# Optimization experiments

Hardware: AMD Instinct MI355X
Metric: run time of the kernel (lower is better)

## Reference

```python
import jax, jax.numpy as jnp
import numpy as np

D, K = 512, 32


def setup_inputs() -> dict:
    key = jax.random.key(0)
    k1, k2, k3 = jax.random.split(key, 3)
    X = jax.random.normal(k1, (8, D, 128, 128), dtype=jnp.float32)
    std1 = 1.0 / (K * D) ** 0.5
    codewords = jax.random.uniform(k2, (K, D), dtype=jnp.float32, minval=-std1, maxval=std1)
    scale = jax.random.uniform(k3, (K,), dtype=jnp.float32, minval=-1.0, maxval=0.0)
    return {"X": X, "codewords": codewords, "scale": scale}


def reference(X, codewords, scale):
    B = X.shape[0]
    # [B, D, H, W] -> [B, N, D]
    Xf = X.reshape(B, D, -1).transpose(0, 2, 1)
    # scaled L2: s_k * ||x_i - d_k||^2, expanded to avoid [B,N,K,D] residuals
    x2 = jnp.sum(Xf * Xf, axis=-1, keepdims=True)            # [B, N, 1]
    c2 = jnp.sum(codewords * codewords, axis=-1)              # [K]
    xc = jnp.einsum('bnd,kd->bnk', Xf, codewords)             # [B, N, K]
    sl = scale * (x2 - 2.0 * xc + c2)                         # [B, N, K]
    A = jax.nn.softmax(sl, axis=2)                            # [B, N, K]
    # E[b,k,d] = sum_n A[b,n,k] * (X[b,n,d] - C[k,d])
    E = jnp.einsum('bnk,bnd->bkd', A, Xf) - jnp.sum(A, axis=1)[..., None] * codewords
    return E
```

## Files before the change

kernel.cpp:

```cpp
#include <hip/hip_runtime.h>
#include <stdint.h>

#define B_ 8
#define D_ 512
#define N_ 16384
#define K_ 32

typedef __attribute__((ext_vector_type(8))) short short8;
typedef __attribute__((ext_vector_type(16))) float f32x16;

union F8 { short8 v; unsigned short s[8]; uint32_t u[4]; uint4 q; };

__device__ __forceinline__ uint32_t bfpack2(float lo, float hi) {
    uint32_t a = __float_as_uint(lo);
    uint32_t b = __float_as_uint(hi);
    a += 0x7FFFu + ((a >> 16) & 1u);
    b += 0x7FFFu + ((b >> 16) & 1u);
    return (a >> 16) | (b & 0xFFFF0000u);
}

__launch_bounds__(256, 2)
__global__ void encode_kernel(const float* __restrict__ X,
                              const float* __restrict__ Cg,
                              const float* __restrict__ scale,
                              float* __restrict__ acc,
                              float* __restrict__ aSumAcc)
{
    __shared__ uint32_t xsTw[D_ * 20];
    __shared__ float    lgp[4][32][33];
    __shared__ uint32_t A_ldsw[K_ * 20];
    __shared__ float4   x2tmp[32][8];
    __shared__ float    mxs[32], invs[32];
    __shared__ float    scs[K_], c2s[K_];
    __shared__ float    c2tmp[K_][9];

    unsigned short* xsTs  = (unsigned short*)xsTw;
    unsigned short* A_lds = (unsigned short*)A_ldsw;

    const int tid = threadIdx.x;
    const int l   = tid & 63;
    const int w   = __builtin_amdgcn_readfirstlane(tid >> 6);
    const int lc  = l & 31;
    const int nh  = l >> 5;
    const int b     = blockIdx.x >> 6;
    const int chunk = blockIdx.x & 63;

    {
        int k = tid >> 3, dg = tid & 7;
        const float* cr = Cg + k * D_ + dg * 64;
        float s2 = 0.f;
#pragma unroll
        for (int i = 0; i < 16; ++i) {
            float4 v = *(const float4*)(cr + i * 4);
            s2 += v.x * v.x + v.y * v.y + v.z * v.z + v.w * v.w;
        }
        c2tmp[k][dg] = s2;
        if (tid < K_) scs[tid] = scale[tid];
    }
    __syncthreads();
    if (tid < K_) {
        float s = 0.f;
#pragma unroll
        for (int dg = 0; dg < 8; ++dg) s += c2tmp[tid][dg];
        c2s[tid] = s;
    }

    F8 cfr[8];
#pragma unroll
    for (int ss = 0; ss < 8; ++ss) {
        int d0 = (8 * w + ss) * 16 + nh * 8;
        const float* cp = Cg + lc * D_ + d0;
        float4 a  = *(const float4*)(cp);
        float4 bq = *(const float4*)(cp + 4);
        cfr[ss].u[0] = bfpack2(a.x, a.y);
        cfr[ss].u[1] = bfpack2(a.z, a.w);
        cfr[ss].u[2] = bfpack2(bq.x, bq.y);
        cfr[ss].u[3] = bfpack2(bq.z, bq.w);
    }

    f32x16 eacc[4];
#pragma unroll
    for (int ti = 0; ti < 4; ++ti)
#pragma unroll
        for (int r = 0; r < 16; ++r) eacc[ti][r] = 0.f;
    float aSumReg = 0.f;

    const int o  = tid >> 3;
    const int nq = tid & 7;
    const size_t xbase = (size_t)b * D_ * N_ + (size_t)chunk * 256;

    for (int t = 0; t < 8; ++t) {
        __syncthreads();

        {
            const float* Xp = X + xbase + t * 32 + nq * 4;
            float4 x2a; x2a.x = x2a.y = x2a.z = x2a.w = 0.f;
#pragma unroll
            for (int r = 0; r < 16; ++r) {
                int d = o + 32 * r;
                float4 v = *(const float4*)(Xp + (size_t)d * N_);
                x2a.x += v.x * v.x; x2a.y += v.y * v.y;
                x2a.z += v.z * v.z; x2a.w += v.w * v.w;
                uint2 p;
                p.x = bfpack2(v.x, v.y);
                p.y = bfpack2(v.z, v.w);
                *(uint2*)&xsTw[d * 20 + nq * 2] = p;
            }
            x2tmp[o][nq] = x2a;
        }
        __syncthreads();

        f32x16 lacc;
#pragma unroll
        for (int r = 0; r < 16; ++r) lacc[r] = 0.f;
#pragma unroll
        for (int ss = 0; ss < 8; ++ss) {
            int d0 = (8 * w + ss) * 16 + nh * 8;
            F8 af;
#pragma unroll
            for (int j = 0; j < 8; ++j)
                af.s[j] = xsTs[(d0 + j) * 40 + lc];
            lacc = __builtin_amdgcn_mfma_f32_32x32x16_bf16(af.v, cfr[ss].v, lacc, 0, 0, 0);
        }
#pragma unroll
        for (int r = 0; r < 16; ++r)
            lgp[w][(r & 3) + 8 * (r >> 2) + 4 * nh][lc] = lacc[r];
        __syncthreads();

        if (w == 0 && l < 32) {
            int n = l;
            float x2v = 0.f;
            const float* xf = (const float*)x2tmp;
#pragma unroll
            for (int oo = 0; oo < 32; ++oo) x2v += xf[oo * 32 + n];
            float lg[K_];
            float m = -3.0e38f;
#pragma unroll
            for (int k = 0; k < K_; ++k) {
                float xc = lgp[0][n][k] + lgp[1][n][k] + lgp[2][n][k] + lgp[3][n][k];
                float sl = scs[k] * (x2v - 2.f * xc + c2s[k]);
                lg[k] = sl;
                m = fmaxf(m, sl);
            }
            float s = 0.f;
#pragma unroll
            for (int k = 0; k < K_; ++k) s += __expf(lg[k] - m);
            mxs[n] = m;
            invs[n] = 1.f / s;
#pragma unroll
            for (int k = 0; k < K_; ++k) lgp[0][n][k] = lg[k];
        }
        __syncthreads();

        if (w == 0) {
            int k = lc;
#pragma unroll
            for (int i = 0; i < 16; i += 2) {
                int n = nh * 16 + i;
                float e0 = __expf(lgp[0][n][k]     - mxs[n])     * invs[n];
                float e1 = __expf(lgp[0][n + 1][k] - mxs[n + 1]) * invs[n + 1];
                aSumReg += e0 + e1;
                A_ldsw[k * 20 + (n >> 1)] = bfpack2(e0, e1);
            }
        }
        __syncthreads();

#pragma unroll
        for (int ti = 0; ti < 4; ++ti) {
            int dcol = (4 * w + ti) * 32 + lc;
#pragma unroll
            for (int ns = 0; ns < 2; ++ns) {
                F8 af, bf;
                af.q = *(const uint4*)&A_lds[lc * 40 + ns * 16 + nh * 8];
                bf.q = *(const uint4*)&xsTs[dcol * 40 + ns * 16 + nh * 8];
                eacc[ti] = __builtin_amdgcn_mfma_f32_32x32x16_bf16(af.v, bf.v, eacc[ti], 0, 0, 0);
            }
        }
    }

    float* accB = acc + (size_t)b * (K_ * D_);
#pragma unroll
    for (int ti = 0; ti < 4; ++ti) {
        int d = (4 * w + ti) * 32 + lc;
#pragma unroll
        for (int r = 0; r < 16; ++r) {
            int k = (r & 3) + 8 * (r >> 2) + 4 * nh;
            unsafeAtomicAdd(&accB[k * D_ + d], eacc[ti][r]);
        }
    }
    if (w == 0) unsafeAtomicAdd(&aSumAcc[b * K_ + lc], aSumReg);
}

__global__ void finish_kernel(const float* __restrict__ acc,
                              const float* __restrict__ aSumAcc,
                              const float* __restrict__ Cg,
                              float* __restrict__ out)
{
    int idx = blockIdx.x * 256 + threadIdx.x;
    int kd = idx & (K_ * D_ - 1);
    int b  = idx >> 14;
    int k  = kd >> 9;
    out[idx] = acc[idx] - aSumAcc[(b << 5) + k] * Cg[kd];
}

extern "C" void kernel_launch(void* const* d_in, const int* in_sizes, int n_in,
                              void* d_out, int out_size, void* d_ws, size_t ws_size,
                              hipStream_t stream)
{
    const float* X  = (const float*)d_in[0];
    const float* C  = (const float*)d_in[1];
    const float* sc = (const float*)d_in[2];
    float* out = (float*)d_out;

    float* acc     = (float*)d_ws;
    float* aSumAcc = acc + B_ * K_ * D_;

    hipMemsetAsync(d_ws, 0, (size_t)(B_ * K_ * D_ + B_ * K_) * sizeof(float), stream);
    encode_kernel<<<B_ * 64, 256, 0, stream>>>(X, C, sc, acc, aSumAcc);
    finish_kernel<<<(B_ * K_ * D_) / 256, 256, 0, stream>>>(acc, aSumAcc, C, out);
}
```

Baseline: 392.9 us.

## Parallelize softmax across all waves and replace global atomics with partial buffers

The softmax step previously ran on a single wave; it is now spread over all four waves, with 8 lanes per row working together through shuffle reductions. The x2 reduction moves from LDS to wave shuffles. The E accumulator no longer uses global float atomics: each block writes a private partial of 64KB, and finish_kernel sums the 64 chunk partials per batch. This removes serial softmax work and atomic contention. In exchange it adds about 32MB of partial-buffer writes and reads.

```diff
diff --git a/kernel.cpp b/kernel.cpp
--- a/kernel.cpp
+++ b/kernel.cpp
@@ -23,16 +23,16 @@
 __global__ void encode_kernel(const float* __restrict__ X,
                               const float* __restrict__ Cg,
                               const float* __restrict__ scale,
-                              float* __restrict__ acc,
+                              float* __restrict__ part,
                               float* __restrict__ aSumAcc)
 {
     __shared__ uint32_t xsTw[D_ * 20];
-    __shared__ float    lgp[4][32][33];
+    __shared__ float    lgp[4][32][36];
     __shared__ uint32_t A_ldsw[K_ * 20];
-    __shared__ float4   x2tmp[32][8];
-    __shared__ float    mxs[32], invs[32];
+    __shared__ float    x2p[4][32];
     __shared__ float    scs[K_], c2s[K_];
     __shared__ float    c2tmp[K_][9];
+    __shared__ float    aSumLds[K_];
 
     unsigned short* xsTs  = (unsigned short*)xsTw;
     unsigned short* A_lds = (unsigned short*)A_ldsw;
@@ -55,7 +55,7 @@
             s2 += v.x * v.x + v.y * v.y + v.z * v.z + v.w * v.w;
         }
         c2tmp[k][dg] = s2;
-        if (tid < K_) scs[tid] = scale[tid];
+        if (tid < K_) { scs[tid] = scale[tid]; aSumLds[tid] = 0.f; }
     }
     __syncthreads();
     if (tid < K_) {
@@ -83,7 +83,12 @@
     for (int ti = 0; ti < 4; ++ti)
 #pragma unroll
         for (int r = 0; r < 16; ++r) eacc[ti][r] = 0.f;
-    float aSumReg = 0.f;
+    float aSumReg[4] = {0.f, 0.f, 0.f, 0.f};
+
+    const int nl  = l >> 3;
+    const int kq  = l & 7;
+    const int smn = w * 8 + nl;
+    const int k0  = kq * 4;
 
     const int o  = tid >> 3;
     const int nq = tid & 7;
@@ -106,7 +111,14 @@
                 p.y = bfpack2(v.z, v.w);
                 *(uint2*)&xsTw[d * 20 + nq * 2] = p;
             }
-            x2tmp[o][nq] = x2a;
+#pragma unroll
+            for (int m = 8; m <= 32; m <<= 1) {
+                x2a.x += __shfl_xor(x2a.x, m);
+                x2a.y += __shfl_xor(x2a.y, m);
+                x2a.z += __shfl_xor(x2a.z, m);
+                x2a.w += __shfl_xor(x2a.w, m);
+            }
+            if (l < 8) *(float4*)&x2p[w][nq * 4] = x2a;
         }
         __syncthreads();
 
@@ -127,41 +139,36 @@
             lgp[w][(r & 3) + 8 * (r >> 2) + 4 * nh][lc] = lacc[r];
         __syncthreads();
 
-        if (w == 0 && l < 32) {
-            int n = l;
-            float x2v = 0.f;
-            const float* xf = (const float*)x2tmp;
-#pragma unroll
-            for (int oo = 0; oo < 32; ++oo) x2v += xf[oo * 32 + n];
-            float lg[K_];
-            float m = -3.0e38f;
-#pragma unroll
-            for (int k = 0; k < K_; ++k) {
-                float xc = lgp[0][n][k] + lgp[1][n][k] + lgp[2][n][k] + lgp[3][n][k];
-                float sl = scs[k] * (x2v - 2.f * xc + c2s[k]);
-                lg[k] = sl;
-                m = fmaxf(m, sl);
-            }
-            float s = 0.f;
-#pragma unroll
-            for (int k = 0; k < K_; ++k) s += __expf(lg[k] - m);
-            mxs[n] = m;
-            invs[n] = 1.f / s;
-#pragma unroll
-            for (int k = 0; k < K_; ++k) lgp[0][n][k] = lg[k];
-        }
-        __syncthreads();
-
-        if (w == 0) {
-            int k = lc;
-#pragma unroll
-            for (int i = 0; i < 16; i += 2) {
-                int n = nh * 16 + i;
-                float e0 = __expf(lgp[0][n][k]     - mxs[n])     * invs[n];
-                float e1 = __expf(lgp[0][n + 1][k] - mxs[n + 1]) * invs[n + 1];
-                aSumReg += e0 + e1;
-                A_ldsw[k * 20 + (n >> 1)] = bfpack2(e0, e1);
-            }
+        {
+            float4 xc = *(const float4*)&lgp[0][smn][k0];
+            float4 x1 = *(const float4*)&lgp[1][smn][k0];
+            float4 x2q = *(const float4*)&lgp[2][smn][k0];
+            float4 x3 = *(const float4*)&lgp[3][smn][k0];
+            xc.x += x1.x + x2q.x + x3.x;
+            xc.y += x1.y + x2q.y + x3.y;
+            xc.z += x1.z + x2q.z + x3.z;
+            xc.w += x1.w + x2q.w + x3.w;
+            float x2v = x2p[0][smn] + x2p[1][smn] + x2p[2][smn] + x2p[3][smn];
+            float sl0 = scs[k0]     * (x2v - 2.f * xc.x + c2s[k0]);
+            float sl1 = scs[k0 + 1] * (x2v - 2.f * xc.y + c2s[k0 + 1]);
+            float sl2 = scs[k0 + 2] * (x2v - 2.f * xc.z + c2s[k0 + 2]);
+            float sl3 = scs[k0 + 3] * (x2v - 2.f * xc.w + c2s[k0 + 3]);
+            float m = fmaxf(fmaxf(sl0, sl1), fmaxf(sl2, sl3));
+#pragma unroll
+            for (int mk = 1; mk <= 4; mk <<= 1) m = fmaxf(m, __shfl_xor(m, mk));
+            float e0 = __expf(sl0 - m), e1 = __expf(sl1 - m);
+            float e2 = __expf(sl2 - m), e3 = __expf(sl3 - m);
+            float s = e0 + e1 + e2 + e3;
+#pragma unroll
+            for (int mk = 1; mk <= 4; mk <<= 1) s += __shfl_xor(s, mk);
+            float inv = 1.f / s;
+            e0 *= inv; e1 *= inv; e2 *= inv; e3 *= inv;
+            aSumReg[0] += e0; aSumReg[1] += e1;
+            aSumReg[2] += e2; aSumReg[3] += e3;
+            A_lds[(k0)     * 40 + smn] = (unsigned short)(bfpack2(e0, 0.f));
+            A_lds[(k0 + 1) * 40 + smn] = (unsigned short)(bfpack2(e1, 0.f));
+            A_lds[(k0 + 2) * 40 + smn] = (unsigned short)(bfpack2(e2, 0.f));
+            A_lds[(k0 + 3) * 40 + smn] = (unsigned short)(bfpack2(e3, 0.f));
         }
         __syncthreads();
 
@@ -178,20 +185,31 @@
         }
     }
 
-    float* accB = acc + (size_t)b * (K_ * D_);
+    float* pB = part + (size_t)blockIdx.x * (K_ * D_);
 #pragma unroll
     for (int ti = 0; ti < 4; ++ti) {
         int d = (4 * w + ti) * 32 + lc;
 #pragma unroll
         for (int r = 0; r < 16; ++r) {
             int k = (r & 3) + 8 * (r >> 2) + 4 * nh;
-            unsafeAtomicAdd(&accB[k * D_ + d], eacc[ti][r]);
-        }
-    }
-    if (w == 0) unsafeAtomicAdd(&aSumAcc[b * K_ + lc], aSumReg);
-}
-
-__global__ void finish_kernel(const float* __restrict__ acc,
+            pB[k * D_ + d] = eacc[ti][r];
+        }
+    }
+
+#pragma unroll
+    for (int i = 0; i < 4; ++i) {
+#pragma unroll
+        for (int m = 8; m <= 32; m <<= 1) aSumReg[i] += __shfl_xor(aSumReg[i], m);
+    }
+    if (l < 8) {
+#pragma unroll
+        for (int i = 0; i < 4; ++i) unsafeAtomicAdd(&aSumLds[k0 + i], aSumReg[i]);
+    }
+    __syncthreads();
+    if (tid < K_) unsafeAtomicAdd(&aSumAcc[b * K_ + tid], aSumLds[tid]);
+}
+
+__global__ void finish_kernel(const float* __restrict__ part,
                               const float* __restrict__ aSumAcc,
                               const float* __restrict__ Cg,
                               float* __restrict__ out)
@@ -200,7 +218,11 @@
     int kd = idx & (K_ * D_ - 1);
     int b  = idx >> 14;
     int k  = kd >> 9;
-    out[idx] = acc[idx] - aSumAcc[(b << 5) + k] * Cg[kd];
+    const float* p = part + (size_t)b * 64 * (K_ * D_) + kd;
+    float s = 0.f;
+#pragma unroll 8
+    for (int c = 0; c < 64; ++c) s += p[(size_t)c * (K_ * D_)];
+    out[idx] = s - aSumAcc[(b << 5) + k] * Cg[kd];
 }
 
 extern "C" void kernel_launch(void* const* d_in, const int* in_sizes, int n_in,
@@ -212,10 +234,10 @@
     const float* sc = (const float*)d_in[2];
     float* out = (float*)d_out;
 
-    float* acc     = (float*)d_ws;
-    float* aSumAcc = acc + B_ * K_ * D_;
-
-    hipMemsetAsync(d_ws, 0, (size_t)(B_ * K_ * D_ + B_ * K_) * sizeof(float), stream);
-    encode_kernel<<<B_ * 64, 256, 0, stream>>>(X, C, sc, acc, aSumAcc);
-    finish_kernel<<<(B_ * K_ * D_) / 256, 256, 0, stream>>>(acc, aSumAcc, C, out);
-}
+    float* part    = (float*)d_ws;
+    float* aSumAcc = part + (size_t)512 * K_ * D_;
+
+    hipMemsetAsync(aSumAcc, 0, B_ * K_ * sizeof(float), stream);
+    encode_kernel<<<B_ * 64, 256, 0, stream>>>(X, C, sc, part, aSumAcc);
+    finish_kernel<<<(B_ * K_ * D_) / 256, 256, 0, stream>>>(part, aSumAcc, C, out);
+}
```

New measurement: 385.4 us. About the same (-1.9%).
